# Performance work log

Hardware: AMD Instinct MI355X
Metric: run time of the kernel (lower is better)

## Reference

```python
import jax, jax.numpy as jnp
import numpy as np

IGNORE_INDEX = -100
N, C = 2097152, 32


def setup_inputs() -> dict:
    key = jax.random.key(0)
    k1, k2, k3 = jax.random.split(key, 3)
    pred = jax.random.normal(k1, (N, C), dtype=jnp.float32)
    # neg_count (~0.95N) > pos_num * factor (~0.15N).
    r = jax.random.randint(k2, (N,), 0, 100, dtype=jnp.int32)
    cls = jax.random.randint(k3, (N,), 1, C, dtype=jnp.int32)
    label = jnp.where(r >= 95, cls, 0).astype(jnp.int32)
    return {"pred": pred, "label": label, "factor": 3}


def reference(pred, label, factor):
    n = pred.shape[0]
    is_pos = label != 0
    pos_num = jnp.sum(is_pos)
    neg_sum = pos_num * factor
    num_neg = n - pos_num

    # max non-background score per row
    pred_value = jnp.max(pred[:, 1:], axis=1)  # [N]

    # descending sort of negative-position scores (positives pushed to the end)
    neg_scores = jnp.where(is_pos, -jnp.inf, pred_value)
    sorted_desc = -jnp.sort(-neg_scores)
    idx = jnp.clip(neg_sum - 1, 0, n - 1)
    threshold = sorted_desc[idx]

    mask_thr = (pred_value >= threshold) | is_pos
    mask_all = label != -1
    mask = jnp.where(num_neg > neg_sum, mask_thr, mask_all)
    mask = jax.lax.stop_gradient(mask)  # torch computes mask on detached numpy

    masked_label = jnp.where(mask, label, IGNORE_INDEX)
    valid = masked_label != IGNORE_INDEX
    safe_label = jnp.where(valid, masked_label, 0)

    logp = jax.nn.log_softmax(pred, axis=-1)  # [N, C]
    nll = -jnp.take_along_axis(logp, safe_label[:, None], axis=1)[:, 0]  # [N]
    denom = jnp.maximum(jnp.sum(valid), 1)
    loss = jnp.sum(jnp.where(valid, nll, 0.0)) / denom.astype(pred.dtype)
    return loss
```

## Files before the change

kernel.cpp:

```cpp
#include <hip/hip_runtime.h>


typedef float f4 __attribute__((ext_vector_type(4)));

#define TILE_ROWS 256
#define ROW_F4    9

struct Ctrl {
    unsigned hist[4][256];
    unsigned pos_num;
    unsigned cnt;
    unsigned bcnt[256];
    float    bsum[256];
    double   sum;
};

__global__ void init_kernel(unsigned* c, int words) {
    for (int i = threadIdx.x + blockIdx.x * blockDim.x; i < words;
         i += blockDim.x * gridDim.x)
        c[i] = 0u;
}

__device__ inline void wave_hist_add(unsigned* h, unsigned bucket) {
    unsigned long long todo = __ballot(1);
    while (todo) {
        int leader = (int)__builtin_ctzll(todo);
        unsigned b = __shfl(bucket, leader);
        unsigned long long same = __ballot(bucket == b) & todo;
        if ((int)(threadIdx.x & 63) == leader)
            atomicAdd(&h[b], (unsigned)__popcll(same));
        todo &= ~same;
    }
}

__global__ void __launch_bounds__(256)
row_kernel(const f4* __restrict__ pred4, const int* __restrict__ label,
           unsigned* __restrict__ keys, float* __restrict__ nll,
           Ctrl* __restrict__ c, int n) {
    __shared__ f4 tile[TILE_ROWS * ROW_F4];
    __shared__ unsigned h[256];
    for (int i = threadIdx.x; i < 256; i += 256) h[i] = 0u;
    __syncthreads();

    const int tid = threadIdx.x;
    int pos_local = 0;
    const int tile_stride = gridDim.x * TILE_ROWS;

    for (int tbase = blockIdx.x * TILE_ROWS; tbase < n; tbase += tile_stride) {
#pragma unroll
        for (int k = 0; k < 8; ++k) {
            int idx = (k << 8) + tid;
            f4 v = pred4[(size_t)tbase * 8 + idx];
            tile[(idx >> 3) * ROW_F4 + (idx & 7)] = v;
        }
        __syncthreads();

        int row = tbase + tid;
        float r[32];
#pragma unroll
        for (int j = 0; j < 8; ++j) {
            f4 v = tile[tid * ROW_F4 + j];
            r[4 * j + 0] = v.x; r[4 * j + 1] = v.y;
            r[4 * j + 2] = v.z; r[4 * j + 3] = v.w;
        }
        float m_nb = r[1];
#pragma unroll
        for (int j = 2; j < 32; ++j) m_nb = fmaxf(m_nb, r[j]);
        float m_all = fmaxf(m_nb, r[0]);

        float s = 0.f;
#pragma unroll
        for (int j = 0; j < 32; ++j) s += __expf(r[j] - m_all);

        int lab = label[row];
        int sl = lab; sl = sl < 0 ? 0 : sl; sl = sl > 31 ? 31 : sl;
        float xl = r[0];
#pragma unroll
        for (int j = 1; j < 32; ++j) xl = (j == sl) ? r[j] : xl;

        nll[row] = (m_all + __logf(s)) - xl;

        bool is_pos = (lab != 0);
        pos_local += is_pos ? 1 : 0;

        float ns = is_pos ? -__builtin_inff() : m_nb;
        unsigned u    = __float_as_uint(ns);
        unsigned ukey = (u & 0x80000000u) ? ~u : (u | 0x80000000u);
        unsigned dkey = ~ukey;
        keys[row] = dkey;
        wave_hist_add(h, dkey >> 24);

        __syncthreads();
    }

#pragma unroll
    for (int off = 32; off > 0; off >>= 1) pos_local += __shfl_down(pos_local, off);
    __shared__ int wsum[4];
    int wid = threadIdx.x >> 6;
    if ((threadIdx.x & 63) == 0) wsum[wid] = pos_local;
    __syncthreads();
    if (threadIdx.x == 0)
        atomicAdd(&c->pos_num, (unsigned)(wsum[0] + wsum[1] + wsum[2] + wsum[3]));

    for (int i = threadIdx.x; i < 256; i += 256)
        if (h[i]) atomicAdd(&c->hist[3][i], h[i]);
}

__device__ void select_chain(const Ctrl* __restrict__ c, int n, int factor,
                             int upto_pass, unsigned& prefix_out,
                             unsigned& rank_out, bool& use_thr_out) {
    __shared__ unsigned s[256];
    __shared__ unsigned sh_byte, sh_rank;
    const int t = threadIdx.x;

    long long pos     = (long long)c->pos_num;
    long long neg_sum = pos * (long long)factor;
    long long num_neg = (long long)n - pos;
    long long idx     = neg_sum - 1;
    if (idx < 0) idx = 0;
    if (idx > (long long)n - 1) idx = (long long)n - 1;
    unsigned rank   = (unsigned)idx;
    unsigned prefix = 0u;

    for (int p = 3; p >= upto_pass; --p) {
        unsigned cnt = c->hist[p][t];
        __syncthreads();
        s[t] = cnt;
        __syncthreads();
#pragma unroll
        for (int off = 1; off < 256; off <<= 1) {
            unsigned v = (t >= off) ? s[t - off] : 0u;
            __syncthreads();
            s[t] += v;
            __syncthreads();
        }
        unsigned incl = s[t], excl = incl - cnt;
        if (cnt > 0u && excl <= rank && rank < incl) {
            sh_byte = (unsigned)t;
            sh_rank = rank - excl;
        }
        __syncthreads();
        prefix |= sh_byte << (8 * p);
        rank = sh_rank;
        __syncthreads();
    }
    prefix_out  = prefix;
    rank_out    = rank;
    use_thr_out = (num_neg > neg_sum);
}

__global__ void __launch_bounds__(256)
hist_kernel(const unsigned* __restrict__ keys, Ctrl* __restrict__ c,
            const int* __restrict__ factor_p, int n, int pass) {
    unsigned prefix, rank; bool use_thr;
    select_chain(c, n, factor_p[0], pass + 1, prefix, rank, use_thr);

    __shared__ unsigned h[256];
    for (int i = threadIdx.x; i < 256; i += 256) h[i] = 0u;
    __syncthreads();

    const unsigned pmask = 0xFFFFFFFFu << (8 * (pass + 1));
    const int shift = 8 * pass;
    const int stride = gridDim.x * blockDim.x;
    for (int i = blockIdx.x * blockDim.x + threadIdx.x; i < n; i += stride) {
        unsigned k = keys[i];
        if ((k & pmask) == prefix) atomicAdd(&h[(k >> shift) & 0xFFu], 1u);
    }
    __syncthreads();
    for (int i = threadIdx.x; i < 256; i += 256)
        if (h[i]) atomicAdd(&c->hist[pass][i], h[i]);
}

__global__ void __launch_bounds__(256)
reduceF_kernel(const unsigned* __restrict__ keys, const int* __restrict__ label,
               const float* __restrict__ nll, Ctrl* __restrict__ c,
               const int* __restrict__ factor_p, int n) {
    unsigned prefix24, rank; bool use_thr;
    select_chain(c, n, factor_p[0], 1, prefix24, rank, use_thr);

    double local = 0.0;
    int cntl = 0;
    const int stride = gridDim.x * blockDim.x;
    for (int i = blockIdx.x * blockDim.x + threadIdx.x; i < n; i += stride) {
        int lab = label[i];
        float nl = nll[i];
        if (use_thr) {
            unsigned k = keys[i];
            unsigned top24 = k & 0xFFFFFF00u;
            bool is_pos = (lab != 0);
            if (is_pos || top24 < prefix24) {
                local += (double)nl; cntl++;
            } else if (top24 == prefix24) {
                unsigned b = k & 0xFFu;
                atomicAdd(&c->bcnt[b], 1u);
                atomicAdd(&c->bsum[b], nl);
            }
        } else {
            if (lab != -1) { local += (double)nl; cntl++; }
        }
    }
#pragma unroll
    for (int off = 32; off > 0; off >>= 1) {
        local += __shfl_down(local, off);
        cntl  += __shfl_down(cntl, off);
    }
    __shared__ double sd[4];
    __shared__ int    si[4];
    int wid = threadIdx.x >> 6;
    if ((threadIdx.x & 63) == 0) { sd[wid] = local; si[wid] = cntl; }
    __syncthreads();
    if (threadIdx.x == 0) {
        atomicAdd(&c->sum, sd[0] + sd[1] + sd[2] + sd[3]);
        atomicAdd(&c->cnt, (unsigned)(si[0] + si[1] + si[2] + si[3]));
    }
}

__global__ void __launch_bounds__(256)
final_kernel(Ctrl* __restrict__ c, const int* __restrict__ factor_p,
             float* __restrict__ out, int n) {
    unsigned prefix, rank; bool use_thr;
    select_chain(c, n, factor_p[0], 1, prefix, rank, use_thr);

    __shared__ unsigned us[256];
    __shared__ float    fs[256];
    __shared__ double   ssum;
    __shared__ unsigned scnt;
    const int t = threadIdx.x;
    if (t == 0) { ssum = 0.0; scnt = 0u; }
    __syncthreads();

    if (use_thr) {
        unsigned bc = c->bcnt[t];
        float    bs = c->bsum[t];
        us[t] = bc; fs[t] = bs;
        __syncthreads();
#pragma unroll
        for (int off = 1; off < 256; off <<= 1) {
            unsigned uv = (t >= off) ? us[t - off] : 0u;
            float    fv = (t >= off) ? fs[t - off] : 0.f;
            __syncthreads();
            us[t] += uv; fs[t] += fv;
            __syncthreads();
        }
        unsigned incl = us[t], excl = incl - bc;
        if (bc > 0u && excl <= rank && rank < incl) {
            ssum = (double)fs[t];
            scnt = incl;
        }
        __syncthreads();
    }
    if (t == 0) {
        double s = c->sum + ssum;
        unsigned ctn = c->cnt + scnt;
        double denom = (ctn == 0u) ? 1.0 : (double)ctn;
        out[0] = (float)(s / denom);
    }
}

extern "C" void kernel_launch(void* const* d_in, const int* in_sizes, int n_in,
                              void* d_out, int out_size, void* d_ws, size_t ws_size,
                              hipStream_t stream) {
    const float* pred = (const float*)d_in[0];
    const int* label  = (const int*)d_in[1];
    const int* factor = (const int*)d_in[2];
    int n = in_sizes[1];
    float* out = (float*)d_out;

    char* ws = (char*)d_ws;
    Ctrl* c = (Ctrl*)ws;
    unsigned* keys = (unsigned*)(ws + 8192);
    float* nll = (float*)(ws + 8192 + (size_t)n * sizeof(unsigned));

    init_kernel<<<2, 256, 0, stream>>>((unsigned*)c, (int)(sizeof(Ctrl) / 4));
    row_kernel<<<2048, 256, 0, stream>>>((const f4*)pred, label, keys, nll, c, n);
    hist_kernel<<<1024, 256, 0, stream>>>(keys, c, factor, n, 2);
    hist_kernel<<<1024, 256, 0, stream>>>(keys, c, factor, n, 1);
    reduceF_kernel<<<2048, 256, 0, stream>>>(keys, label, nll, c, factor, n);
    final_kernel<<<1, 256, 0, stream>>>(c, factor, out, n);
}
```

Measured before the change: 139.7 us.

## Replace multi-pass radix select with global 20-bit histogram and fused final reduction

The row kernel now also builds a 1M-bin global histogram over the top 20 key bits with per-element atomics. This lets the reduce kernel find the threshold prefix directly, so the two extra histogram passes over the keys go away. Boundary elements are compacted into a pairs buffer instead of going through per-bucket global atomics. The last block to finish then does the final bucket select and reduction, removing the separate final kernel. The cost is 4 MB of extra zeroing and heavy contended global atomics in the row kernel.

```diff
diff --git a/kernel.cpp b/kernel.cpp
--- a/kernel.cpp
+++ b/kernel.cpp
@@ -7,18 +7,21 @@
 #define ROW_F4    9
 
 struct Ctrl {
-    unsigned hist[4][256];
+    unsigned hist8[256];
     unsigned pos_num;
     unsigned cnt;
-    unsigned bcnt[256];
-    float    bsum[256];
+    unsigned done;
+    unsigned pair_cnt;
     double   sum;
 };
 
-__global__ void init_kernel(unsigned* c, int words) {
+#define HIST20_OFF  4096
+#define HIST20_SZ   (1u << 20)
+
+__global__ void init_kernel(unsigned* w, int words) {
     for (int i = threadIdx.x + blockIdx.x * blockDim.x; i < words;
          i += blockDim.x * gridDim.x)
-        c[i] = 0u;
+        w[i] = 0u;
 }
 
 __device__ inline void wave_hist_add(unsigned* h, unsigned bucket) {
@@ -36,7 +39,7 @@
 __global__ void __launch_bounds__(256)
 row_kernel(const f4* __restrict__ pred4, const int* __restrict__ label,
            unsigned* __restrict__ keys, float* __restrict__ nll,
-           Ctrl* __restrict__ c, int n) {
+           unsigned* __restrict__ hist20, Ctrl* __restrict__ c, int n) {
     __shared__ f4 tile[TILE_ROWS * ROW_F4];
     __shared__ unsigned h[256];
     for (int i = threadIdx.x; i < 256; i += 256) h[i] = 0u;
@@ -89,6 +92,7 @@
         unsigned dkey = ~ukey;
         keys[row] = dkey;
         wave_hist_add(h, dkey >> 24);
+        if (!is_pos) atomicAdd(&hist20[dkey >> 12], 1u);
 
         __syncthreads();
     }
@@ -103,29 +107,32 @@
         atomicAdd(&c->pos_num, (unsigned)(wsum[0] + wsum[1] + wsum[2] + wsum[3]));
 
     for (int i = threadIdx.x; i < 256; i += 256)
-        if (h[i]) atomicAdd(&c->hist[3][i], h[i]);
-}
-
-__device__ void select_chain(const Ctrl* __restrict__ c, int n, int factor,
-                             int upto_pass, unsigned& prefix_out,
-                             unsigned& rank_out, bool& use_thr_out) {
+        if (h[i]) atomicAdd(&c->hist8[i], h[i]);
+}
+
+__global__ void __launch_bounds__(256)
+reduceF_kernel(const unsigned* __restrict__ keys, const int* __restrict__ label,
+               const float* __restrict__ nll, const unsigned* __restrict__ hist20,
+               unsigned long long* __restrict__ pairs, Ctrl* __restrict__ c,
+               const int* __restrict__ factor_p, int n, float* __restrict__ out) {
     __shared__ unsigned s[256];
-    __shared__ unsigned sh_byte, sh_rank;
+    __shared__ unsigned shb, shr;
     const int t = threadIdx.x;
+    const int lane = t & 63;
 
     long long pos     = (long long)c->pos_num;
-    long long neg_sum = pos * (long long)factor;
+    long long neg_sum = pos * (long long)factor_p[0];
     long long num_neg = (long long)n - pos;
     long long idx     = neg_sum - 1;
     if (idx < 0) idx = 0;
     if (idx > (long long)n - 1) idx = (long long)n - 1;
-    unsigned rank   = (unsigned)idx;
-    unsigned prefix = 0u;
-
-    for (int p = 3; p >= upto_pass; --p) {
-        unsigned cnt = c->hist[p][t];
-        __syncthreads();
-        s[t] = cnt;
+    const bool use_thr = (num_neg > neg_sum);
+
+    unsigned prefix20 = 0u, rank2 = 0u;
+    if (use_thr) {
+        unsigned rank = (unsigned)idx;
+        unsigned cnt8 = c->hist8[t];
+        s[t] = cnt8;
         __syncthreads();
 #pragma unroll
         for (int off = 1; off < 256; off <<= 1) {
@@ -134,69 +141,71 @@
             s[t] += v;
             __syncthreads();
         }
-        unsigned incl = s[t], excl = incl - cnt;
-        if (cnt > 0u && excl <= rank && rank < incl) {
-            sh_byte = (unsigned)t;
-            sh_rank = rank - excl;
-        }
-        __syncthreads();
-        prefix |= sh_byte << (8 * p);
-        rank = sh_rank;
-        __syncthreads();
-    }
-    prefix_out  = prefix;
-    rank_out    = rank;
-    use_thr_out = (num_neg > neg_sum);
-}
-
-__global__ void __launch_bounds__(256)
-hist_kernel(const unsigned* __restrict__ keys, Ctrl* __restrict__ c,
-            const int* __restrict__ factor_p, int n, int pass) {
-    unsigned prefix, rank; bool use_thr;
-    select_chain(c, n, factor_p[0], pass + 1, prefix, rank, use_thr);
-
-    __shared__ unsigned h[256];
-    for (int i = threadIdx.x; i < 256; i += 256) h[i] = 0u;
-    __syncthreads();
-
-    const unsigned pmask = 0xFFFFFFFFu << (8 * (pass + 1));
-    const int shift = 8 * pass;
-    const int stride = gridDim.x * blockDim.x;
-    for (int i = blockIdx.x * blockDim.x + threadIdx.x; i < n; i += stride) {
-        unsigned k = keys[i];
-        if ((k & pmask) == prefix) atomicAdd(&h[(k >> shift) & 0xFFu], 1u);
-    }
-    __syncthreads();
-    for (int i = threadIdx.x; i < 256; i += 256)
-        if (h[i]) atomicAdd(&c->hist[pass][i], h[i]);
-}
-
-__global__ void __launch_bounds__(256)
-reduceF_kernel(const unsigned* __restrict__ keys, const int* __restrict__ label,
-               const float* __restrict__ nll, Ctrl* __restrict__ c,
-               const int* __restrict__ factor_p, int n) {
-    unsigned prefix24, rank; bool use_thr;
-    select_chain(c, n, factor_p[0], 1, prefix24, rank, use_thr);
+        unsigned incl = s[t], excl = incl - cnt8;
+        if (cnt8 > 0u && excl <= rank && rank < incl) {
+            shb = (unsigned)t;
+            shr = rank - excl;
+        }
+        __syncthreads();
+        unsigned b3 = shb;
+        unsigned rank1 = shr;
+        __syncthreads();
+
+        const unsigned* slice = hist20 + ((size_t)b3 << 12);
+        unsigned lc[16]; unsigned lsum = 0u;
+#pragma unroll
+        for (int i = 0; i < 16; ++i) { lc[i] = slice[t * 16 + i]; lsum += lc[i]; }
+        s[t] = lsum;
+        __syncthreads();
+#pragma unroll
+        for (int off = 1; off < 256; off <<= 1) {
+            unsigned v = (t >= off) ? s[t - off] : 0u;
+            __syncthreads();
+            s[t] += v;
+            __syncthreads();
+        }
+        unsigned incl2 = s[t], excl2 = incl2 - lsum;
+        if (lsum > 0u && excl2 <= rank1 && rank1 < incl2) {
+            unsigned r = rank1 - excl2;
+#pragma unroll
+            for (int i = 0; i < 16; ++i) {
+                if (r < lc[i]) { shb = (unsigned)(t * 16 + i); shr = r; break; }
+                r -= lc[i];
+            }
+        }
+        __syncthreads();
+        prefix20 = (b3 << 12) | shb;
+        rank2 = shr;
+        __syncthreads();
+    }
 
     double local = 0.0;
     int cntl = 0;
     const int stride = gridDim.x * blockDim.x;
-    for (int i = blockIdx.x * blockDim.x + threadIdx.x; i < n; i += stride) {
+    for (int i = blockIdx.x * blockDim.x + t; i < n; i += stride) {
         int lab = label[i];
         float nl = nll[i];
+        bool doapp = false;
+        unsigned k = 0u;
         if (use_thr) {
-            unsigned k = keys[i];
-            unsigned top24 = k & 0xFFFFFF00u;
+            k = keys[i];
+            unsigned top20 = k >> 12;
             bool is_pos = (lab != 0);
-            if (is_pos || top24 < prefix24) {
-                local += (double)nl; cntl++;
-            } else if (top24 == prefix24) {
-                unsigned b = k & 0xFFu;
-                atomicAdd(&c->bcnt[b], 1u);
-                atomicAdd(&c->bsum[b], nl);
-            }
+            if (is_pos || top20 < prefix20) { local += (double)nl; cntl++; }
+            else if (top20 == prefix20) doapp = true;
         } else {
             if (lab != -1) { local += (double)nl; cntl++; }
+        }
+        unsigned long long m = __ballot(doapp);
+        if (doapp) {
+            int lead = (int)__builtin_ctzll(m);
+            unsigned base = 0u;
+            if (lane == lead) base = atomicAdd(&c->pair_cnt, (unsigned)__popcll(m));
+            base = __shfl(base, lead);
+            unsigned off = (unsigned)__popcll(m & ((1ull << lane) - 1ull));
+            pairs[base + off] =
+                ((unsigned long long)(k & 0xFFFu) << 32) |
+                (unsigned long long)__float_as_uint(nl);
         }
     }
 #pragma unroll
@@ -206,54 +215,82 @@
     }
     __shared__ double sd[4];
     __shared__ int    si[4];
-    int wid = threadIdx.x >> 6;
-    if ((threadIdx.x & 63) == 0) { sd[wid] = local; si[wid] = cntl; }
+    int wid = t >> 6;
+    if (lane == 0) { sd[wid] = local; si[wid] = cntl; }
     __syncthreads();
-    if (threadIdx.x == 0) {
+    __shared__ int s_last;
+    if (t == 0) {
         atomicAdd(&c->sum, sd[0] + sd[1] + sd[2] + sd[3]);
         atomicAdd(&c->cnt, (unsigned)(si[0] + si[1] + si[2] + si[3]));
-    }
-}
-
-__global__ void __launch_bounds__(256)
-final_kernel(Ctrl* __restrict__ c, const int* __restrict__ factor_p,
-             float* __restrict__ out, int n) {
-    unsigned prefix, rank; bool use_thr;
-    select_chain(c, n, factor_p[0], 1, prefix, rank, use_thr);
-
-    __shared__ unsigned us[256];
-    __shared__ float    fs[256];
-    __shared__ double   ssum;
-    __shared__ unsigned scnt;
-    const int t = threadIdx.x;
-    if (t == 0) { ssum = 0.0; scnt = 0u; }
+        __threadfence();
+        unsigned d = atomicAdd(&c->done, 1u);
+        s_last = (d == gridDim.x - 1) ? 1 : 0;
+    }
     __syncthreads();
+    if (!s_last) return;
+
+    __threadfence();
+    __shared__ unsigned pc[4096];
+    __shared__ float    ps[4096];
+    __shared__ double   fssum;
+    __shared__ unsigned fscnt;
+    if (t == 0) { fssum = 0.0; fscnt = 0u; }
 
     if (use_thr) {
-        unsigned bc = c->bcnt[t];
-        float    bs = c->bsum[t];
-        us[t] = bc; fs[t] = bs;
+        for (int i = t; i < 4096; i += 256) { pc[i] = 0u; ps[i] = 0.f; }
+        __syncthreads();
+        unsigned M = c->pair_cnt;
+        for (unsigned j = t; j < M; j += 256) {
+            unsigned long long p = pairs[j];
+            unsigned b = (unsigned)(p >> 32);
+            atomicAdd(&pc[b], 1u);
+            atomicAdd(&ps[b], __uint_as_float((unsigned)p));
+        }
+        __syncthreads();
+        unsigned lc2[16]; unsigned lsum = 0u;
+#pragma unroll
+        for (int i = 0; i < 16; ++i) { lc2[i] = pc[t * 16 + i]; lsum += lc2[i]; }
+        s[t] = lsum;
         __syncthreads();
 #pragma unroll
         for (int off = 1; off < 256; off <<= 1) {
-            unsigned uv = (t >= off) ? us[t - off] : 0u;
-            float    fv = (t >= off) ? fs[t - off] : 0.f;
-            __syncthreads();
-            us[t] += uv; fs[t] += fv;
-            __syncthreads();
-        }
-        unsigned incl = us[t], excl = incl - bc;
-        if (bc > 0u && excl <= rank && rank < incl) {
-            ssum = (double)fs[t];
-            scnt = incl;
+            unsigned v = (t >= off) ? s[t - off] : 0u;
+            __syncthreads();
+            s[t] += v;
+            __syncthreads();
+        }
+        unsigned incl = s[t], excl = incl - lsum;
+        if (lsum > 0u && excl <= rank2 && rank2 < incl) {
+            unsigned r = rank2 - excl;
+#pragma unroll
+            for (int i = 0; i < 16; ++i) {
+                if (r < lc2[i]) { shb = (unsigned)(t * 16 + i); break; }
+                r -= lc2[i];
+            }
+        }
+        __syncthreads();
+        unsigned bstar = shb;
+        double fsl = 0.0; unsigned fcl = 0u;
+        for (int i = t; i < 4096; i += 256)
+            if ((unsigned)i <= bstar) { fcl += pc[i]; fsl += (double)ps[i]; }
+#pragma unroll
+        for (int off = 32; off > 0; off >>= 1) {
+            fsl += __shfl_down(fsl, off);
+            fcl += __shfl_down(fcl, off);
+        }
+        if (lane == 0) { sd[wid] = fsl; si[wid] = (int)fcl; }
+        __syncthreads();
+        if (t == 0) {
+            fssum = sd[0] + sd[1] + sd[2] + sd[3];
+            fscnt = (unsigned)(si[0] + si[1] + si[2] + si[3]);
         }
         __syncthreads();
     }
     if (t == 0) {
-        double s = c->sum + ssum;
-        unsigned ctn = c->cnt + scnt;
+        double sum = c->sum + fssum;
+        unsigned ctn = c->cnt + fscnt;
         double denom = (ctn == 0u) ? 1.0 : (double)ctn;
-        out[0] = (float)(s / denom);
+        out[0] = (float)(sum / denom);
     }
 }
 
@@ -268,13 +305,16 @@
 
     char* ws = (char*)d_ws;
     Ctrl* c = (Ctrl*)ws;
-    unsigned* keys = (unsigned*)(ws + 8192);
-    float* nll = (float*)(ws + 8192 + (size_t)n * sizeof(unsigned));
-
-    init_kernel<<<2, 256, 0, stream>>>((unsigned*)c, (int)(sizeof(Ctrl) / 4));
-    row_kernel<<<2048, 256, 0, stream>>>((const f4*)pred, label, keys, nll, c, n);
-    hist_kernel<<<1024, 256, 0, stream>>>(keys, c, factor, n, 2);
-    hist_kernel<<<1024, 256, 0, stream>>>(keys, c, factor, n, 1);
-    reduceF_kernel<<<2048, 256, 0, stream>>>(keys, label, nll, c, factor, n);
-    final_kernel<<<1, 256, 0, stream>>>(c, factor, out, n);
-}
+    unsigned* hist20 = (unsigned*)(ws + HIST20_OFF);
+    unsigned* keys = (unsigned*)(ws + HIST20_OFF + HIST20_SZ * 4);
+    float* nll = (float*)(ws + HIST20_OFF + HIST20_SZ * 4 + (size_t)n * 4);
+    unsigned long long* pairs =
+        (unsigned long long*)(ws + HIST20_OFF + HIST20_SZ * 4 + (size_t)n * 8);
+
+    int zwords = (int)((HIST20_OFF + HIST20_SZ * 4) / 4);
+    init_kernel<<<1024, 256, 0, stream>>>((unsigned*)ws, zwords);
+    row_kernel<<<2048, 256, 0, stream>>>((const f4*)pred, label, keys, nll,
+                                         hist20, c, n);
+    reduceF_kernel<<<1024, 256, 0, stream>>>(keys, label, nll, hist20, pairs,
+                                             c, factor, n, out);
+}
```

After: 420.4 us. 3.01x slower.
